# Optimization experiments

Hardware: AMD Instinct MI355X
Metric: run time of the kernel (lower is better)

Reference implementation:

```python
import jax, jax.numpy as jnp
import numpy as np

N = 10000
H_INPUTS = 128
H = 512
RW_LEN = 16
BATCH = 512


def setup_inputs() -> dict:
    key = jax.random.key(0)
    ks = jax.random.split(key, 5)
    x = jax.random.normal(ks[0], (BATCH, RW_LEN, N + 1), dtype=jnp.float32)
    # xavier-ish scaled params
    W_down = jax.random.normal(ks[1], (N, H_INPUTS), dtype=jnp.float32) * (1.0 / np.sqrt(N))
    W_cell = jax.random.normal(ks[2], (H_INPUTS + 1 + H, 4 * H), dtype=jnp.float32) * (1.0 / np.sqrt(H_INPUTS + 1 + H))
    b_cell = jnp.zeros((4 * H,), dtype=jnp.float32)
    W_out = jax.random.normal(ks[3], (H, 1), dtype=jnp.float32) * (1.0 / np.sqrt(H))
    b_out = jnp.zeros((1,), dtype=jnp.float32)
    return {"x": x, "W_down": W_down, "W_cell": W_cell, "b_cell": b_cell,
            "W_out": W_out, "b_out": b_out}


def _forward(x, W_down, W_cell, b_cell, W_out, b_out):
    B = x.shape[0]
    x_rw = x[:, :, :N]                       # [B, T, N]
    x_weights = x[:, :, -1:]                 # [B, T, 1]
    xa = jnp.einsum('btn,nh->bth', x_rw, W_down)  # down-projection [B, T, H_in]
    xc = jnp.concatenate([xa, x_weights], axis=2)  # [B, T, H_in+1]
    xc_t = jnp.swapaxes(xc, 0, 1)            # [T, B, H_in+1] for scan

    h0 = jnp.zeros((B, H), dtype=x.dtype)
    c0 = jnp.zeros((B, H), dtype=x.dtype)

    def step(carry, xt):
        h, c = carry
        gates = jnp.concatenate([xt, h], axis=1) @ W_cell + b_cell  # [B, 4H]
        i_g, c_g, f_g, o_g = jnp.split(gates, 4, axis=1)
        # custom forget-gate bias of +1
        c_new = c * jax.nn.sigmoid(f_g + 1.0) + jax.nn.sigmoid(i_g) * jnp.tanh(c_g)
        h_new = jax.nn.sigmoid(o_g) * jnp.tanh(c_new)
        return (h_new, c_new), None

    (h, _), _ = jax.lax.scan(step, (h0, c0), xc_t)
    pred = h @ W_out + b_out                 # [B, 1]
    return pred


def reference(x, W_down, W_cell, b_cell, W_out, b_out):
    return _forward(x, W_down, W_cell, b_cell, W_out, b_out)
```

## Files before the change

kernel.cpp:

```cpp
#include <hip/hip_runtime.h>
#include <cmath>

#define TID ((int)threadIdx.x)

typedef __bf16 bf16_t;
typedef bf16_t bf16x8 __attribute__((ext_vector_type(8)));
typedef float floatx4 __attribute__((ext_vector_type(4)));

#define MFMA(a, b, c) __builtin_amdgcn_mfma_f32_16x16x32_bf16(a, b, c, 0, 0, 0)

constexpr int N_IN = 10000;
constexpr int XP   = 10001;
constexpr int KPD  = 10240;
constexpr int HH   = 512;
constexpr int TT   = 16;
constexpr int NB   = 512;
constexpr int MROW = 8192;
constexpr int KSPLIT = 16;
constexpr int KCHUNK = 640;
constexpr int KT_A = 10;

__device__ __forceinline__ float sigm(float x) { return 1.0f / (1.0f + expf(-x)); }

__device__ __forceinline__ void gload16(const void* g, void* lds) {
  __builtin_amdgcn_global_load_lds(
      (const __attribute__((address_space(1))) unsigned int*)g,
      (__attribute__((address_space(3))) unsigned int*)lds, 16, 0, 0);
}

__global__ __launch_bounds__(256)
void kPrepWd(const float* __restrict__ Wd, bf16_t* __restrict__ Whi, bf16_t* __restrict__ Wlo) {
  __shared__ float Ts[64][133];
  const int k0 = blockIdx.x * 64;
  #pragma unroll
  for (int i = 0; i < 32; ++i) {
    int f = TID + 256 * i;
    int kk = f >> 7, c = f & 127;
    int k = k0 + kk;
    Ts[kk][c] = (k < N_IN) ? Wd[(size_t)k * 128 + c] : 0.0f;
  }
  __syncthreads();
  const int lane = TID & 63, w = TID >> 6;
  for (int pass = 0; pass < 32; ++pass) {
    int c = pass * 4 + w;
    float v = Ts[lane][c];
    bf16_t hi = (bf16_t)v;
    bf16_t lo = (bf16_t)(v - (float)hi);
    Whi[(size_t)c * KPD + k0 + lane] = hi;
    Wlo[(size_t)c * KPD + k0 + lane] = lo;
  }
}

__global__ __launch_bounds__(256)
void kPrepWc(const float* __restrict__ Wc, bf16_t* __restrict__ Wxh, bf16_t* __restrict__ Wxl,
             float* __restrict__ wN, bf16_t* __restrict__ Whh, bf16_t* __restrict__ Whl) {
  __shared__ float Ts[64][133];
  const int k0 = blockIdx.x * 64;
  const int c0 = blockIdx.y * 128;
  #pragma unroll
  for (int i = 0; i < 32; ++i) {
    int f = TID + 256 * i;
    int kk = f >> 7, cc = f & 127;
    int k = k0 + kk;
    Ts[kk][cc] = (k < 641) ? Wc[(size_t)k * 2048 + c0 + cc] : 0.0f;
  }
  __syncthreads();
  const int lane = TID & 63, w = TID >> 6;
  const int k = k0 + lane;
  for (int pass = 0; pass < 32; ++pass) {
    int cc = pass * 4 + w;
    int c = c0 + cc;
    float v = Ts[lane][cc];
    bf16_t hi = (bf16_t)v;
    bf16_t lo = (bf16_t)(v - (float)hi);
    if (k < 128) {
      Wxh[(size_t)c * 128 + k] = hi;
      Wxl[(size_t)c * 128 + k] = lo;
    } else if (k == 128) {
      wN[c] = v;
    } else if (k < 641) {
      Whh[(size_t)c * 512 + (k - 129)] = hi;
      Whl[(size_t)c * 512 + (k - 129)] = lo;
    }
  }
}

__global__ __launch_bounds__(256)
void kPrepXw(const float* __restrict__ x, float* __restrict__ xw) {
  int r = blockIdx.x * 256 + TID;
  xw[r] = x[(size_t)r * XP + N_IN];
}

__global__ __launch_bounds__(256, 2)
void kA_mfma(const float* __restrict__ x, const bf16_t* __restrict__ Whi,
             const bf16_t* __restrict__ Wlo, float* __restrict__ parts) {
  __shared__ __align__(16) bf16_t Bt[2][2048 * 8];
  const int lane = TID & 63, w = TID >> 6;
  const int row0 = blockIdx.x * 128 + w * 32;
  const int kbase = blockIdx.y * KCHUNK;
  floatx4 acc[2][8] = {};

  auto STAGE = [&](int buf, int kt) {
    const int k0 = kbase + kt * 64;
    #pragma unroll
    for (int i = 0; i < 8; ++i) {
      int L = i * 256 + TID;
      int arr = L >> 10, col = (L >> 3) & 127, g = L & 7;
      int gs = g ^ (col & 7);
      const bf16_t* src = (arr ? Wlo : Whi) + (size_t)col * KPD + k0 + gs * 8;
      gload16(src, &Bt[buf][(size_t)L * 8]);
    }
  };
  auto LOADX = [&](float4 (&xb)[2][2][2], int kt) {
    const int k0 = kbase + kt * 64;
    #pragma unroll
    for (int rf = 0; rf < 2; ++rf) {
      const float* xp = x + (size_t)(row0 + rf * 16 + (lane & 15)) * XP;
      #pragma unroll
      for (int h = 0; h < 2; ++h) {
        int kk0 = k0 + h * 32 + (lane >> 4) * 8;
        if (kk0 < N_IN) {
          xb[rf][h][0] = *(const float4*)(xp + kk0);
          xb[rf][h][1] = *(const float4*)(xp + kk0 + 4);
        } else {
          xb[rf][h][0] = make_float4(0.f, 0.f, 0.f, 0.f);
          xb[rf][h][1] = make_float4(0.f, 0.f, 0.f, 0.f);
        }
      }
    }
  };
  auto COMPUTE = [&](int buf, const float4 (&xb)[2][2][2]) {
    #pragma unroll
    for (int h = 0; h < 2; ++h) {
      const int p = h * 4 + (lane >> 4);
      bf16x8 ahi[2], alo[2];
      #pragma unroll
      for (int rf = 0; rf < 2; ++rf) {
        float vv[8] = {xb[rf][h][0].x, xb[rf][h][0].y, xb[rf][h][0].z, xb[rf][h][0].w,
                       xb[rf][h][1].x, xb[rf][h][1].y, xb[rf][h][1].z, xb[rf][h][1].w};
        #pragma unroll
        for (int e = 0; e < 8; ++e) {
          bf16_t hi = (bf16_t)vv[e];
          ahi[rf][e] = hi;
          alo[rf][e] = (bf16_t)(vv[e] - (float)hi);
        }
      }
      #pragma unroll
      for (int cf = 0; cf < 8; ++cf) {
        const int col = cf * 16 + (lane & 15);
        const int g = p ^ (col & 7);
        bf16x8 bhi = *(const bf16x8*)&Bt[buf][(col * 8 + g) * 8];
        bf16x8 blo = *(const bf16x8*)&Bt[buf][(1024 + col * 8 + g) * 8];
        #pragma unroll
        for (int rf = 0; rf < 2; ++rf) {
          acc[rf][cf] = MFMA(ahi[rf], bhi, acc[rf][cf]);
          acc[rf][cf] = MFMA(ahi[rf], blo, acc[rf][cf]);
          acc[rf][cf] = MFMA(alo[rf], bhi, acc[rf][cf]);
        }
      }
    }
  };

  float4 xbA[2][2][2], xbB[2][2][2];
  STAGE(0, 0);
  LOADX(xbA, 0);
  __syncthreads();
  #pragma unroll
  for (int kt = 0; kt < KT_A; kt += 2) {
    if (kt + 1 < KT_A) { STAGE(1, kt + 1); LOADX(xbB, kt + 1); }
    COMPUTE(0, xbA);
    __syncthreads();
    if (kt + 2 < KT_A) { STAGE(0, kt + 2); LOADX(xbA, kt + 2); }
    COMPUTE(1, xbB);
    __syncthreads();
  }

  float* dst = parts + (size_t)blockIdx.y * MROW * 128;
  #pragma unroll
  for (int rf = 0; rf < 2; ++rf)
    #pragma unroll
    for (int cf = 0; cf < 8; ++cf)
      #pragma unroll
      for (int r = 0; r < 4; ++r) {
        int row = row0 + rf * 16 + (lane >> 4) * 4 + r;
        int col = cf * 16 + (lane & 15);
        dst[(size_t)row * 128 + col] = acc[rf][cf][r];
      }
}

__global__ __launch_bounds__(256)
void kRed(const float* __restrict__ parts, float* __restrict__ xa) {
  size_t i4 = ((size_t)blockIdx.x * 256 + TID) * 4;
  float4 v = make_float4(0.f, 0.f, 0.f, 0.f);
  #pragma unroll
  for (int s = 0; s < KSPLIT; ++s) {
    float4 p = *(const float4*)&parts[(size_t)s * MROW * 128 + i4];
    v.x += p.x; v.y += p.y; v.z += p.z; v.w += p.w;
  }
  *(float4*)&xa[i4] = v;
}

__global__ __launch_bounds__(512, 2)
void kGx(const float* __restrict__ xa, const float* __restrict__ xw,
         const bf16_t* __restrict__ Wxh, const bf16_t* __restrict__ Wxl,
         const float* __restrict__ wN, const float* __restrict__ bc,
         float* __restrict__ gx) {
  __shared__ __align__(16) bf16_t Bt[4096 * 8];
  const int lane = TID & 63, w = TID >> 6;
  const int wr = w & 3, wc = w >> 2;
  const int rowbase = blockIdx.x * 128 + wr * 32;
  const int JB = blockIdx.y * 32;
  floatx4 acc[2][4] = {};

  #pragma unroll
  for (int i = 0; i < 8; ++i) {
    int L = i * 512 + TID;
    int arr = L >> 11, ce = (L >> 4) & 127, g = L & 15;
    int gs = g ^ (ce & 15);
    int c_src = (ce & 3) * 512 + JB + (ce >> 2);
    const bf16_t* src = (arr ? Wxl : Wxh) + (size_t)c_src * 128 + gs * 8;
    gload16(src, &Bt[(size_t)L * 8]);
  }
  float4 xb[2][2][2][2];
  #pragma unroll
  for (int kt = 0; kt < 2; ++kt)
    #pragma unroll
    for (int rf = 0; rf < 2; ++rf) {
      const float* ap = xa + (size_t)(rowbase + rf * 16 + (lane & 15)) * 128;
      #pragma unroll
      for (int h = 0; h < 2; ++h) {
        int kk0 = kt * 64 + h * 32 + (lane >> 4) * 8;
        xb[kt][rf][h][0] = *(const float4*)(ap + kk0);
        xb[kt][rf][h][1] = *(const float4*)(ap + kk0 + 4);
      }
    }
  __syncthreads();
  #pragma unroll
  for (int kt = 0; kt < 2; ++kt) {
    #pragma unroll
    for (int h = 0; h < 2; ++h) {
      const int p = kt * 8 + h * 4 + (lane >> 4);
      bf16x8 ahi[2], alo[2];
      #pragma unroll
      for (int rf = 0; rf < 2; ++rf) {
        float vv[8] = {xb[kt][rf][h][0].x, xb[kt][rf][h][0].y, xb[kt][rf][h][0].z, xb[kt][rf][h][0].w,
                       xb[kt][rf][h][1].x, xb[kt][rf][h][1].y, xb[kt][rf][h][1].z, xb[kt][rf][h][1].w};
        #pragma unroll
        for (int e = 0; e < 8; ++e) {
          bf16_t hi = (bf16_t)vv[e];
          ahi[rf][e] = hi;
          alo[rf][e] = (bf16_t)(vv[e] - (float)hi);
        }
      }
      #pragma unroll
      for (int cf = 0; cf < 4; ++cf) {
        const int ce = wc * 64 + cf * 16 + (lane & 15);
        const int g = p ^ (ce & 15);
        bf16x8 bhi = *(const bf16x8*)&Bt[(ce * 16 + g) * 8];
        bf16x8 blo = *(const bf16x8*)&Bt[(2048 + ce * 16 + g) * 8];
        #pragma unroll
        for (int rf = 0; rf < 2; ++rf) {
          acc[rf][cf] = MFMA(ahi[rf], bhi, acc[rf][cf]);
          acc[rf][cf] = MFMA(ahi[rf], blo, acc[rf][cf]);
          acc[rf][cf] = MFMA(alo[rf], bhi, acc[rf][cf]);
        }
      }
    }
  }
  #pragma unroll
  for (int rf = 0; rf < 2; ++rf)
    #pragma unroll
    for (int cf = 0; cf < 4; ++cf) {
      const int ce = wc * 64 + cf * 16 + (lane & 15);
      const int n = blockIdx.y * 128 + ce;
      const int c_src = (ce & 3) * 512 + JB + (ce >> 2);
      const float bias = bc[c_src];
      const float wn = wN[c_src];
      #pragma unroll
      for (int r = 0; r < 4; ++r) {
        int row = rowbase + rf * 16 + (lane >> 4) * 4 + r;
        gx[(size_t)row * 2048 + n] = acc[rf][cf][r] + bias + xw[row] * wn;
      }
    }
}

__global__ __launch_bounds__(128, 2)
void kStepH(const bf16_t* __restrict__ hhi_in, const bf16_t* __restrict__ hlo_in,
            const bf16_t* __restrict__ Whh, const bf16_t* __restrict__ Whl,
            const float* __restrict__ gx, const float* __restrict__ c_in,
            bf16_t* __restrict__ hhi_out, bf16_t* __restrict__ hlo_out,
            float* __restrict__ c_out, int t, int has_h) {
  __shared__ __align__(16) bf16_t Bt[2][1024 * 8];
  const int lane = TID & 63, w = TID >> 6;
  const int j0 = blockIdx.x * 16;
  const int brow0 = blockIdx.y * 32 + w * 16;
  floatx4 acc[4] = {};

  auto STAGE = [&](int buf, int kt) {
    const int k0 = kt * 64;
    #pragma unroll
    for (int i = 0; i < 8; ++i) {
      int L = i * 128 + TID;
      int arr = L >> 9, ce = (L >> 3) & 63, g = L & 7;
      int gs = g ^ (ce & 7);
      int c_src = (ce >> 4) * 512 + j0 + (ce & 15);
      const bf16_t* src = (arr ? Whl : Whh) + (size_t)c_src * 512 + k0 + gs * 8;
      gload16(src, &Bt[buf][(size_t)L * 8]);
    }
  };
  auto LOADA = [&](bf16x8 (&ar)[2][2], int kt) {
    const int b = brow0 + (lane & 15);
    #pragma unroll
    for (int h = 0; h < 2; ++h) {
      const int kk0 = kt * 64 + h * 32 + (lane >> 4) * 8;
      ar[h][0] = *(const bf16x8*)&hhi_in[(size_t)b * HH + kk0];
      ar[h][1] = *(const bf16x8*)&hlo_in[(size_t)b * HH + kk0];
    }
  };
  auto COMPUTE = [&](int buf, const bf16x8 (&ar)[2][2]) {
    #pragma unroll
    for (int h = 0; h < 2; ++h) {
      const int p = h * 4 + (lane >> 4);
      #pragma unroll
      for (int cf = 0; cf < 4; ++cf) {
        const int ce = cf * 16 + (lane & 15);
        const int g = p ^ (ce & 7);
        bf16x8 bhi = *(const bf16x8*)&Bt[buf][(ce * 8 + g) * 8];
        bf16x8 blo = *(const bf16x8*)&Bt[buf][(512 + ce * 8 + g) * 8];
        acc[cf] = MFMA(ar[h][0], bhi, acc[cf]);
        acc[cf] = MFMA(ar[h][0], blo, acc[cf]);
        acc[cf] = MFMA(ar[h][1], bhi, acc[cf]);
      }
    }
  };

  if (has_h) {
    bf16x8 aA[2][2], aB[2][2];
    STAGE(0, 0);
    LOADA(aA, 0);
    __syncthreads();
    #pragma unroll
    for (int kt = 0; kt < 8; kt += 2) {
      if (kt + 1 < 8) { STAGE(1, kt + 1); LOADA(aB, kt + 1); }
      COMPUTE(0, aA);
      __syncthreads();
      if (kt + 2 < 8) { STAGE(0, kt + 2); LOADA(aA, kt + 2); }
      COMPUTE(1, aB);
      __syncthreads();
    }
  }

  const int j = j0 + (lane & 15);
  #pragma unroll
  for (int r = 0; r < 4; ++r) {
    int b = brow0 + (lane >> 4) * 4 + r;
    float4 gv = *(const float4*)&gx[((size_t)b * TT + t) * 2048 + (size_t)j * 4];
    float gi = acc[0][r] + gv.x;
    float gc = acc[1][r] + gv.y;
    float gf = acc[2][r] + gv.z;
    float go = acc[3][r] + gv.w;
    float cp = has_h ? c_in[(size_t)b * HH + j] : 0.0f;
    float cn = cp * sigm(gf + 1.0f) + sigm(gi) * tanhf(gc);
    float hn = sigm(go) * tanhf(cn);
    c_out[(size_t)b * HH + j] = cn;
    bf16_t hh = (bf16_t)hn;
    hhi_out[(size_t)b * HH + j] = hh;
    hlo_out[(size_t)b * HH + j] = (bf16_t)(hn - (float)hh);
  }
}

__global__ __launch_bounds__(64)
void kC_out(const bf16_t* __restrict__ hh, const bf16_t* __restrict__ hl,
            const float* __restrict__ Wo, const float* __restrict__ bo,
            float* __restrict__ out) {
  const int b = blockIdx.x;
  float s = 0.0f;
  for (int j = TID; j < HH; j += 64)
    s += ((float)hh[(size_t)b * HH + j] + (float)hl[(size_t)b * HH + j]) * Wo[j];
  #pragma unroll
  for (int off = 32; off > 0; off >>= 1) s += __shfl_down(s, off);
  if (TID == 0) out[b] = s + bo[0];
}

extern "C" void kernel_launch(void* const* d_in, const int* in_sizes, int n_in,
                              void* d_out, int out_size, void* d_ws, size_t ws_size,
                              hipStream_t stream) {
  const float* x  = (const float*)d_in[0];
  const float* Wd = (const float*)d_in[1];
  const float* Wc = (const float*)d_in[2];
  const float* bc = (const float*)d_in[3];
  const float* Wo = (const float*)d_in[4];
  const float* bo = (const float*)d_in[5];
  float* out = (float*)d_out;

  char* wsb = (char*)d_ws;
  size_t off = 0;
  auto alloc = [&](size_t bytes) -> void* {
    void* p = wsb + off;
    off = (off + bytes + 255) & ~(size_t)255;
    return p;
  };
  bf16_t* WdThi = (bf16_t*)alloc((size_t)128 * KPD * 2);
  bf16_t* WdTlo = (bf16_t*)alloc((size_t)128 * KPD * 2);
  bf16_t* WxThi = (bf16_t*)alloc((size_t)2048 * 128 * 2);
  bf16_t* WxTlo = (bf16_t*)alloc((size_t)2048 * 128 * 2);
  bf16_t* WhThi = (bf16_t*)alloc((size_t)2048 * 512 * 2);
  bf16_t* WhTlo = (bf16_t*)alloc((size_t)2048 * 512 * 2);
  float*  wN    = (float*)alloc(2048 * 4);
  float*  xw    = (float*)alloc(MROW * 4);
  float*  xa    = (float*)alloc((size_t)MROW * 128 * 4);
  float*  parts = (float*)alloc((size_t)KSPLIT * MROW * 128 * 4);
  float*  gx    = parts;
  bf16_t* h0hi = (bf16_t*)alloc((size_t)NB * HH * 2);
  bf16_t* h0lo = (bf16_t*)alloc((size_t)NB * HH * 2);
  bf16_t* h1hi = (bf16_t*)alloc((size_t)NB * HH * 2);
  bf16_t* h1lo = (bf16_t*)alloc((size_t)NB * HH * 2);
  float*  c0   = (float*)alloc((size_t)NB * HH * 4);
  float*  c1   = (float*)alloc((size_t)NB * HH * 4);
  bf16_t* hhi[2] = {h0hi, h1hi};
  bf16_t* hlo[2] = {h0lo, h1lo};
  float*  cb[2]  = {c0, c1};

  kPrepWd<<<160, 256, 0, stream>>>(Wd, WdThi, WdTlo);
  kPrepWc<<<dim3(11, 16), 256, 0, stream>>>(Wc, WxThi, WxTlo, wN, WhThi, WhTlo);
  kPrepXw<<<32, 256, 0, stream>>>(x, xw);
  kA_mfma<<<dim3(64, KSPLIT), 256, 0, stream>>>(x, WdThi, WdTlo, parts);
  kRed<<<1024, 256, 0, stream>>>(parts, xa);
  kGx<<<dim3(64, 16), 512, 0, stream>>>(xa, xw, WxThi, WxTlo, wN, bc, gx);
  for (int t = 0; t < TT; ++t) {
    kStepH<<<dim3(32, 16), 128, 0, stream>>>(hhi[t & 1], hlo[t & 1], WhThi, WhTlo,
        gx, cb[t & 1], hhi[(t + 1) & 1], hlo[(t + 1) & 1], cb[(t + 1) & 1],
        t, (t == 0) ? 0 : 1);
  }
  kC_out<<<512, 64, 0, stream>>>(h0hi, h0lo, Wo, bo, out);
}
```

Baseline: 403.3 us.

## Halve K-split, fold xw gather into kGx, single-wave recurrent step blocks

The down-projection K-split drops from 16 to 8, so there are fewer partial buffers to reduce in kRed. The separate kPrepXw launch is removed and kGx reads the last x column directly. kStepH now runs one wavefront per block with twice as many blocks, and it replaces __syncthreads with explicit vmcnt waits on the LDS-direct loads. This cuts launch count, block barriers and reduction traffic, at the cost of less parallelism in kA and more redundant weight staging per step.

```diff
diff --git a/kernel.cpp b/kernel.cpp
--- a/kernel.cpp
+++ b/kernel.cpp
@@ -16,9 +16,9 @@
 constexpr int TT   = 16;
 constexpr int NB   = 512;
 constexpr int MROW = 8192;
-constexpr int KSPLIT = 16;
-constexpr int KCHUNK = 640;
-constexpr int KT_A = 10;
+constexpr int KSPLIT = 8;
+constexpr int KCHUNK = 1280;
+constexpr int KT_A = 20;
 
 __device__ __forceinline__ float sigm(float x) { return 1.0f / (1.0f + expf(-x)); }
 
@@ -85,12 +85,6 @@
   }
 }
 
-__global__ __launch_bounds__(256)
-void kPrepXw(const float* __restrict__ x, float* __restrict__ xw) {
-  int r = blockIdx.x * 256 + TID;
-  xw[r] = x[(size_t)r * XP + N_IN];
-}
-
 __global__ __launch_bounds__(256, 2)
 void kA_mfma(const float* __restrict__ x, const bf16_t* __restrict__ Whi,
              const bf16_t* __restrict__ Wlo, float* __restrict__ parts) {
@@ -201,7 +195,7 @@
 }
 
 __global__ __launch_bounds__(512, 2)
-void kGx(const float* __restrict__ xa, const float* __restrict__ xw,
+void kGx(const float* __restrict__ xa, const float* __restrict__ x,
          const bf16_t* __restrict__ Wxh, const bf16_t* __restrict__ Wxl,
          const float* __restrict__ wN, const float* __restrict__ bc,
          float* __restrict__ gx) {
@@ -279,28 +273,29 @@
       #pragma unroll
       for (int r = 0; r < 4; ++r) {
         int row = rowbase + rf * 16 + (lane >> 4) * 4 + r;
-        gx[(size_t)row * 2048 + n] = acc[rf][cf][r] + bias + xw[row] * wn;
-      }
-    }
-}
-
-__global__ __launch_bounds__(128, 2)
+        float xwv = x[(size_t)row * XP + N_IN];
+        gx[(size_t)row * 2048 + n] = acc[rf][cf][r] + bias + xwv * wn;
+      }
+    }
+}
+
+__global__ __launch_bounds__(64)
 void kStepH(const bf16_t* __restrict__ hhi_in, const bf16_t* __restrict__ hlo_in,
             const bf16_t* __restrict__ Whh, const bf16_t* __restrict__ Whl,
             const float* __restrict__ gx, const float* __restrict__ c_in,
             bf16_t* __restrict__ hhi_out, bf16_t* __restrict__ hlo_out,
             float* __restrict__ c_out, int t, int has_h) {
   __shared__ __align__(16) bf16_t Bt[2][1024 * 8];
-  const int lane = TID & 63, w = TID >> 6;
+  const int lane = TID;
   const int j0 = blockIdx.x * 16;
-  const int brow0 = blockIdx.y * 32 + w * 16;
+  const int brow0 = blockIdx.y * 16;
   floatx4 acc[4] = {};
 
   auto STAGE = [&](int buf, int kt) {
     const int k0 = kt * 64;
     #pragma unroll
-    for (int i = 0; i < 8; ++i) {
-      int L = i * 128 + TID;
+    for (int i = 0; i < 16; ++i) {
+      int L = i * 64 + lane;
       int arr = L >> 9, ce = (L >> 3) & 63, g = L & 7;
       int gs = g ^ (ce & 7);
       int c_src = (ce >> 4) * 512 + j0 + (ce & 15);
@@ -338,15 +333,22 @@
     bf16x8 aA[2][2], aB[2][2];
     STAGE(0, 0);
     LOADA(aA, 0);
-    __syncthreads();
     #pragma unroll
     for (int kt = 0; kt < 8; kt += 2) {
-      if (kt + 1 < 8) { STAGE(1, kt + 1); LOADA(aB, kt + 1); }
+      if (kt + 1 < 8) {
+        STAGE(1, kt + 1); LOADA(aB, kt + 1);
+        asm volatile("s_waitcnt vmcnt(20)" ::: "memory");
+      } else {
+        asm volatile("s_waitcnt vmcnt(0)" ::: "memory");
+      }
       COMPUTE(0, aA);
-      __syncthreads();
-      if (kt + 2 < 8) { STAGE(0, kt + 2); LOADA(aA, kt + 2); }
+      if (kt + 2 < 8) {
+        STAGE(0, kt + 2); LOADA(aA, kt + 2);
+        asm volatile("s_waitcnt vmcnt(20)" ::: "memory");
+      } else {
+        asm volatile("s_waitcnt vmcnt(0)" ::: "memory");
+      }
       COMPUTE(1, aB);
-      __syncthreads();
     }
   }
 
@@ -407,10 +409,9 @@
   bf16_t* WhThi = (bf16_t*)alloc((size_t)2048 * 512 * 2);
   bf16_t* WhTlo = (bf16_t*)alloc((size_t)2048 * 512 * 2);
   float*  wN    = (float*)alloc(2048 * 4);
-  float*  xw    = (float*)alloc(MROW * 4);
   float*  xa    = (float*)alloc((size_t)MROW * 128 * 4);
-  float*  parts = (float*)alloc((size_t)KSPLIT * MROW * 128 * 4);
-  float*  gx    = parts;
+  float*  gx    = (float*)alloc((size_t)MROW * 2048 * 4);
+  float*  parts = gx;
   bf16_t* h0hi = (bf16_t*)alloc((size_t)NB * HH * 2);
   bf16_t* h0lo = (bf16_t*)alloc((size_t)NB * HH * 2);
   bf16_t* h1hi = (bf16_t*)alloc((size_t)NB * HH * 2);
@@ -423,12 +424,11 @@
 
   kPrepWd<<<160, 256, 0, stream>>>(Wd, WdThi, WdTlo);
   kPrepWc<<<dim3(11, 16), 256, 0, stream>>>(Wc, WxThi, WxTlo, wN, WhThi, WhTlo);
-  kPrepXw<<<32, 256, 0, stream>>>(x, xw);
   kA_mfma<<<dim3(64, KSPLIT), 256, 0, stream>>>(x, WdThi, WdTlo, parts);
   kRed<<<1024, 256, 0, stream>>>(parts, xa);
-  kGx<<<dim3(64, 16), 512, 0, stream>>>(xa, xw, WxThi, WxTlo, wN, bc, gx);
+  kGx<<<dim3(64, 16), 512, 0, stream>>>(xa, x, WxThi, WxTlo, wN, bc, gx);
   for (int t = 0; t < TT; ++t) {
-    kStepH<<<dim3(32, 16), 128, 0, stream>>>(hhi[t & 1], hlo[t & 1], WhThi, WhTlo,
+    kStepH<<<dim3(32, 32), 64, 0, stream>>>(hhi[t & 1], hlo[t & 1], WhThi, WhTlo,
         gx, cb[t & 1], hhi[(t + 1) & 1], hlo[(t + 1) & 1], cb[(t + 1) & 1],
         t, (t == 0) ? 0 : 1);
   }
```

Result: slower. 433.6 us (+7.5%).
